# Optimization experiments

Measured on AMD Instinct MI355X. Metric: run time of the kernel, lower is better.

Reference implementation:

```python
import jax, jax.numpy as jnp
import numpy as np

L = 4


def make_coord(h, w):
    # pixel-center coords in [-1,1], shape (h*w, 2), dim order (y, x)
    ys = -1.0 + 1.0 / h + (2.0 / h) * jnp.arange(h, dtype=jnp.float32)
    xs = -1.0 + 1.0 / w + (2.0 / w) * jnp.arange(w, dtype=jnp.float32)
    gy, gx = jnp.meshgrid(ys, xs, indexing='ij')
    return jnp.stack([gy, gx], axis=-1).reshape(-1, 2)


def bilinear_sample(feat, gx, gy):
    # feat: (B,C,H,W); gx,gy in [-1,1], shape (B,N); align_corners=True
    B, C, H, W = feat.shape
    ix = (gx + 1.0) * 0.5 * (W - 1)
    iy = (gy + 1.0) * 0.5 * (H - 1)
    x0f = jnp.floor(ix)
    y0f = jnp.floor(iy)
    x0 = jnp.clip(x0f.astype(jnp.int32), 0, W - 1)
    x1 = jnp.clip(x0 + 1, 0, W - 1)
    y0 = jnp.clip(y0f.astype(jnp.int32), 0, H - 1)
    y1 = jnp.clip(y0 + 1, 0, H - 1)
    wx1 = ix - x0f
    wx0 = 1.0 - wx1
    wy1 = iy - y0f
    wy0 = 1.0 - wy1
    featf = feat.reshape(B, C, H * W)

    def g(yi, xi):
        idx = yi * W + xi  # (B,N)
        return jnp.take_along_axis(featf, idx[:, None, :], axis=2)  # (B,C,N)

    out = (g(y0, x0) * (wy0 * wx0)[:, None, :] + g(y0, x1) * (wy0 * wx1)[:, None, :]
           + g(y1, x0) * (wy1 * wx0)[:, None, :] + g(y1, x1) * (wy1 * wx1)[:, None, :])
    return out.transpose(0, 2, 1)  # (B,N,C)


def pos_enc(x):
    # x: (B,N,2) -> (B,N,4L); per dim: [sin_0..sin_{L-1}, cos_0..cos_{L-1}]
    freq = (2.0 ** jnp.arange(L, dtype=jnp.float32)) * np.pi
    spec = x[..., None] * freq  # (B,N,2,L)
    enc = jnp.concatenate([jnp.sin(spec), jnp.cos(spec)], axis=-1)  # (B,N,2,2L)
    return enc.reshape(*x.shape[:-1], 4 * L)


def mlp(x, w0, b0, w1, b1, w2, b2, w3, b3):
    h = jax.nn.relu(x @ w0 + b0)
    h = jax.nn.relu(h @ w1 + b1)
    h = jax.nn.relu(h @ w2 + b2)
    return h @ w3 + b3


def setup_inputs() -> dict:
    key = jax.random.key(0)
    ks = jax.random.split(key, 8)
    B, C, H, W = 4, 64, 128, 128
    hid, out_dim = 256, 3
    in_dim = C + 2 + 4 * L + 2  # 84
    s = 0.05
    return {
        'inp': jax.random.normal(ks[0], (B, C, H, W), jnp.float32),
        'w0': jax.random.normal(ks[1], (in_dim, hid), jnp.float32) * s,
        'b0': jnp.zeros((hid,), jnp.float32),
        'w1': jax.random.normal(ks[2], (hid, hid), jnp.float32) * s,
        'b1': jnp.zeros((hid,), jnp.float32),
        'w2': jax.random.normal(ks[3], (hid, hid), jnp.float32) * s,
        'b2': jnp.zeros((hid,), jnp.float32),
        'w3': jax.random.normal(ks[4], (hid, out_dim), jnp.float32) * s,
        'b3': jnp.zeros((out_dim,), jnp.float32),
        'scale': 2,
    }


def reference(inp, w0, b0, w1, b1, w2, b2, w3, b3, scale):
    B, C, H, W = inp.shape
    th, tw = int(round(H * scale)), int(round(W * scale))
    N = th * tw
    coord = jnp.broadcast_to(make_coord(th, tw)[None], (B, N, 2))
    # cell = (2/th, 2/tw); rel_cell = cell * (H, W)
    rel_cell = jnp.broadcast_to(
        jnp.array([2.0 / th * H, 2.0 / tw * W], jnp.float32), (B, N, 2))
    # feature-pixel coordinate map, appended as extra channels so one gather serves both
    fc = make_coord(H, W).reshape(H, W, 2).transpose(2, 0, 1)  # (2,H,W)
    aug = jnp.concatenate([inp, jnp.broadcast_to(fc[None], (B, 2, H, W))], axis=1)

    pe = pos_enc(coord)  # same for all 4 ensemble branches
    hw_scale = jnp.array([H, W], jnp.float32)
    rx, ry = 1.0 / H, 1.0 / W
    eps = 1e-6

    preds, areas = [], []
    for vx in (-1, 1):
        for vy in (-1, 1):
            c0 = jnp.clip(coord[..., 0] + vx * rx + eps, -1 + 1e-6, 1 - 1e-6)
            c1 = jnp.clip(coord[..., 1] + vy * ry + eps, -1 + 1e-6, 1 - 1e-6)
            # grid_sample uses (x, y) = flipped coord -> gx=c1, gy=c0
            q = bilinear_sample(aug, c1, c0)  # (B,N,C+2)
            q_feat, q_coord = q[..., :C], q[..., C:]
            rel = (coord - q_coord) * hw_scale  # (B,N,2)
            x = jnp.concatenate([q_feat, rel, pe, rel_cell], axis=-1)
            preds.append(mlp(x, w0, b0, w1, b1, w2, b2, w3, b3))
            areas.append(jnp.abs(rel[..., 0] * rel[..., 1]) + 1e-9)

    areas = [areas[3], areas[2], areas[1], areas[0]]  # diagonal swap
    tot = areas[0] + areas[1] + areas[2] + areas[3]
    ret = sum(p * (a / tot)[..., None] for p, a in zip(preds, areas))  # (B,N,out)
    return ret.reshape(B, th, tw, -1).transpose(0, 3, 1, 2)  # (B,out,th,tw)
```

## Files before the change

kernel.cpp:

```cpp
#include <hip/hip_runtime.h>
#include <math.h>

#define NB 4
#define NH 128
#define NW 128
#define TH 256
#define TW 256
#define K0 96
#define MROWS 256
#define PIXB 64

typedef _Float16 f16;
typedef f16  f16x8 __attribute__((ext_vector_type(8)));
typedef f16  f16x4v __attribute__((ext_vector_type(4)));
typedef float f32x4 __attribute__((ext_vector_type(4)));
typedef float f32x16 __attribute__((ext_vector_type(16)));

#define OFF_W1 24576
#define OFF_W2 (OFF_W1 + 65536)
#define OFF_W3 (OFF_W2 + 65536)
#define OFF_PE (OFF_W3 + 4096)
#define WS_W_ELEMS (OFF_PE + 4096)
#define FT_ELEMS (NB * NH * NW * 64)

__device__ __forceinline__ int act_off(int row, int colByte) {
  return row * 512 + (colByte ^ ((row & 7) << 4));
}

__device__ __forceinline__ void gload_lds16(const f16* g, f16* l) {
  __builtin_amdgcn_global_load_lds(
      (const __attribute__((address_space(1))) void*)(g),
      (__attribute__((address_space(3))) void*)(l), 16, 0, 0);
}

__global__ void cvt_weights(const float* __restrict__ w0, const float* __restrict__ w1,
                            const float* __restrict__ w2, const float* __restrict__ w3,
                            f16* __restrict__ ws) {
  const int i = blockIdx.x * 256 + threadIdx.x;
  if (i < 24576) {
    const int n = i / 96, k = i - n * 96;
    ws[i] = (k < 84) ? (f16)w0[k * 256 + n] : (f16)0.f;
  } else if (i < OFF_W2) {
    const int j = i - OFF_W1; const int n = j >> 8, k = j & 255;
    ws[i] = (f16)w1[k * 256 + n];
  } else if (i < OFF_W3) {
    const int j = i - OFF_W2; const int n = j >> 8, k = j & 255;
    ws[i] = (f16)w2[k * 256 + n];
  } else if (i < OFF_PE) {
    const int j = i - OFF_W3; const int n = j >> 8, k = j & 255;
    ws[i] = (n < 3) ? (f16)w3[k * 3 + n] : (f16)0.f;
  } else if (i < WS_W_ELEMS) {
    const int j = i - OFF_PE;
    const int o = (j & 2047) >> 3, e = j & 7;
    const float c = (2.0f * o + 1.0f) / 256.0f - 1.0f;
    const float f = (float)(1 << (e & 3)) * (float)M_PI;
    ws[i] = (f16)((e < 4) ? sinf(c * f) : cosf(c * f));
  }
}

__global__ void transpose_feat(const float* __restrict__ feat, f16* __restrict__ ft) {
  __shared__ f16 tile[64][66];
  const int bid = blockIdx.x;
  const int xt = bid & 1, y = (bid >> 1) & 127, b = bid >> 8;
  const int x0 = xt * 64;
  {
    const int c4 = threadIdx.x >> 6, x = threadIdx.x & 63;
#pragma unroll
    for (int co = 0; co < 16; ++co) {
      const int c = co * 4 + c4;
      tile[x][c] = (f16)feat[((size_t)(b * 64 + c) * NH + y) * NW + x0 + x];
    }
  }
  __syncthreads();
  {
    const int x4 = threadIdx.x >> 6, c = threadIdx.x & 63;
#pragma unroll
    for (int xo = 0; xo < 16; ++xo) {
      const int x = xo * 4 + x4;
      ft[((size_t)(b * NH + y) * NW + x0 + x) * 64 + c] = tile[x][c];
    }
  }
}

template<int K>
__device__ __forceinline__ void dense_layer(const f16* __restrict__ Wt,
                                            const float* __restrict__ bias,
                                            char* actc, f16* wlds,
                                            int wm, int wn, int l, int tid) {
  constexpr int NK = K / 16, NP = NK / 2;
  const int lo = l & 31, hi = l >> 5;
  const int sn = tid & 255, sh = tid >> 8;
  const f16* src = Wt + (size_t)sn * K + sh * 8;
  f16* wdst = wlds + sh * 2048 + ((tid >> 6) & 3) * 512;
  const int aoff = (wn * 64 + lo) * 8;
  const int brow0 = wm * 128 + lo;

  f32x16 acc[2][4];
#pragma unroll
  for (int nt = 0; nt < 2; ++nt) {
    f32x16 ci;
#pragma unroll
    for (int g = 0; g < 4; ++g) {
      const float4 b4 = *(const float4*)(bias + wn * 64 + nt * 32 + 8 * g + 4 * hi);
      ci[4 * g + 0] = b4.x; ci[4 * g + 1] = b4.y; ci[4 * g + 2] = b4.z; ci[4 * g + 3] = b4.w;
    }
#pragma unroll
    for (int mt = 0; mt < 4; ++mt) acc[nt][mt] = ci;
  }

  gload_lds16(src + 0 * 16, wdst + 0 * 4096);
  gload_lds16(src + 1 * 16, wdst + 1 * 4096);
  asm volatile("s_waitcnt vmcnt(0)" ::: "memory");
  __builtin_amdgcn_s_barrier();
  asm volatile("" ::: "memory");

#pragma unroll
  for (int p = 0; p < NP; ++p) {
    const int s0 = 2 * p, s1 = 2 * p + 1;
    if (p + 1 < NP) {
      gload_lds16(src + (s0 + 2) * 16, wdst + ((s0 + 2) & 3) * 4096);
      gload_lds16(src + (s1 + 2) * 16, wdst + ((s1 + 2) & 3) * 4096);
    }
    const f16* wb0 = wlds + (s0 & 3) * 4096 + hi * 2048 + aoff;
    const f16x8 A00 = *(const f16x8*)(wb0);
    const f16x8 A01 = *(const f16x8*)(wb0 + 256);
    const f16x8 B00 = *(const f16x8*)(actc + act_off(brow0 + 0 * 32, s0 * 32 + hi * 16));
    const f16x8 B01 = *(const f16x8*)(actc + act_off(brow0 + 1 * 32, s0 * 32 + hi * 16));
    const f16x8 B02 = *(const f16x8*)(actc + act_off(brow0 + 2 * 32, s0 * 32 + hi * 16));
    const f16x8 B03 = *(const f16x8*)(actc + act_off(brow0 + 3 * 32, s0 * 32 + hi * 16));
    const f16* wb1 = wlds + (s1 & 3) * 4096 + hi * 2048 + aoff;
    const f16x8 A10 = *(const f16x8*)(wb1);
    const f16x8 A11 = *(const f16x8*)(wb1 + 256);
    const f16x8 B10 = *(const f16x8*)(actc + act_off(brow0 + 0 * 32, s1 * 32 + hi * 16));
    const f16x8 B11 = *(const f16x8*)(actc + act_off(brow0 + 1 * 32, s1 * 32 + hi * 16));
    const f16x8 B12 = *(const f16x8*)(actc + act_off(brow0 + 2 * 32, s1 * 32 + hi * 16));
    const f16x8 B13 = *(const f16x8*)(actc + act_off(brow0 + 3 * 32, s1 * 32 + hi * 16));

    asm volatile("s_waitcnt lgkmcnt(6)" ::: "memory");
    __builtin_amdgcn_sched_barrier(0);
    __builtin_amdgcn_s_setprio(1);
    acc[0][0] = __builtin_amdgcn_mfma_f32_32x32x16_f16(A00, B00, acc[0][0], 0, 0, 0);
    acc[0][1] = __builtin_amdgcn_mfma_f32_32x32x16_f16(A00, B01, acc[0][1], 0, 0, 0);
    acc[0][2] = __builtin_amdgcn_mfma_f32_32x32x16_f16(A00, B02, acc[0][2], 0, 0, 0);
    acc[0][3] = __builtin_amdgcn_mfma_f32_32x32x16_f16(A00, B03, acc[0][3], 0, 0, 0);
    acc[1][0] = __builtin_amdgcn_mfma_f32_32x32x16_f16(A01, B00, acc[1][0], 0, 0, 0);
    acc[1][1] = __builtin_amdgcn_mfma_f32_32x32x16_f16(A01, B01, acc[1][1], 0, 0, 0);
    acc[1][2] = __builtin_amdgcn_mfma_f32_32x32x16_f16(A01, B02, acc[1][2], 0, 0, 0);
    acc[1][3] = __builtin_amdgcn_mfma_f32_32x32x16_f16(A01, B03, acc[1][3], 0, 0, 0);
    __builtin_amdgcn_s_setprio(0);

    asm volatile("s_waitcnt lgkmcnt(0)" ::: "memory");
    __builtin_amdgcn_sched_barrier(0);
    __builtin_amdgcn_s_setprio(1);
    acc[0][0] = __builtin_amdgcn_mfma_f32_32x32x16_f16(A10, B10, acc[0][0], 0, 0, 0);
    acc[0][1] = __builtin_amdgcn_mfma_f32_32x32x16_f16(A10, B11, acc[0][1], 0, 0, 0);
    acc[0][2] = __builtin_amdgcn_mfma_f32_32x32x16_f16(A10, B12, acc[0][2], 0, 0, 0);
    acc[0][3] = __builtin_amdgcn_mfma_f32_32x32x16_f16(A10, B13, acc[0][3], 0, 0, 0);
    acc[1][0] = __builtin_amdgcn_mfma_f32_32x32x16_f16(A11, B10, acc[1][0], 0, 0, 0);
    acc[1][1] = __builtin_amdgcn_mfma_f32_32x32x16_f16(A11, B11, acc[1][1], 0, 0, 0);
    acc[1][2] = __builtin_amdgcn_mfma_f32_32x32x16_f16(A11, B12, acc[1][2], 0, 0, 0);
    acc[1][3] = __builtin_amdgcn_mfma_f32_32x32x16_f16(A11, B13, acc[1][3], 0, 0, 0);
    __builtin_amdgcn_s_setprio(0);

    if (p + 1 < NP)
      asm volatile("s_waitcnt vmcnt(0)" ::: "memory");
    __builtin_amdgcn_s_barrier();
    asm volatile("" ::: "memory");
  }

#pragma unroll
  for (int nt = 0; nt < 2; ++nt)
#pragma unroll
    for (int mt = 0; mt < 4; ++mt)
#pragma unroll
      for (int g = 0; g < 4; ++g) {
        f16x4v o;
        o[0] = (f16)fmaxf(acc[nt][mt][4 * g + 0], 0.f);
        o[1] = (f16)fmaxf(acc[nt][mt][4 * g + 1], 0.f);
        o[2] = (f16)fmaxf(acc[nt][mt][4 * g + 2], 0.f);
        o[3] = (f16)fmaxf(acc[nt][mt][4 * g + 3], 0.f);
        const int row = wm * 128 + mt * 32 + lo;
        const int colB = wn * 128 + nt * 64 + 16 * g + 8 * hi;
        *(f16x4v*)(actc + act_off(row, colB)) = o;
      }
}

template<bool USE_FT>
__global__ __launch_bounds__(512, 2) void inr2d_mfma(
    const float* __restrict__ feat, const f16* __restrict__ ft,
    const float* __restrict__ b0, const float* __restrict__ b1,
    const float* __restrict__ b2, const float* __restrict__ b3,
    const f16* __restrict__ ws, float* __restrict__ out)
{
  __shared__ f16 act[MROWS * 256];
  __shared__ f16 wlds[4 * 4096];
  f16 (*pred_s)[4] = (f16(*)[4])wlds;

  char* actc = (char*)act;
  const int t = threadIdx.x;
  const int blk = ((blockIdx.x & 7) << 9) | (blockIdx.x >> 3);

  {
    const int r = t >> 1, sub = t & 1;
    const int pix = r >> 2, e = r & 3;
    const int gp = blk * PIXB + pix;
    const int b = gp >> 16, rem = gp & 65535;
    const int oy = rem >> 8, ox = rem & 255;

    const float cy = (2.0f * oy + 1.0f) / (float)TH - 1.0f;
    const float cx = (2.0f * ox + 1.0f) / (float)TW - 1.0f;
    const float vx = (e & 2) ? 1.0f : -1.0f;
    const float vy = (e & 1) ? 1.0f : -1.0f;
    const float rr = 1.0f / (float)NH;

    float c0 = fminf(fmaxf(cy + vx * rr + 1e-6f, -1.0f + 1e-6f), 1.0f - 1e-6f);
    float c1 = fminf(fmaxf(cx + vy * rr + 1e-6f, -1.0f + 1e-6f), 1.0f - 1e-6f);

    const float ix = (c1 + 1.0f) * 0.5f * (float)(NW - 1);
    const float iy = (c0 + 1.0f) * 0.5f * (float)(NH - 1);
    const float x0f = floorf(ix), y0f = floorf(iy);
    int x0 = (int)x0f; x0 = max(0, min(x0, NW - 1));
    int x1 = min(x0 + 1, NW - 1);
    int y0 = (int)y0f; y0 = max(0, min(y0, NH - 1));
    int y1 = min(y0 + 1, NH - 1);
    const float wx1 = ix - x0f, wx0 = 1.0f - wx1;
    const float wy1 = iy - y0f, wy0 = 1.0f - wy1;
    const float w00 = wy0 * wx0, w01 = wy0 * wx1, w10 = wy1 * wx0, w11 = wy1 * wx1;

    if (USE_FT) {
      const f16* fb = ft + (size_t)b * (NH * NW * 64);
      const f16* r00 = fb + (size_t)(y0 * NW + x0) * 64 + sub * 32;
      const f16* r01 = fb + (size_t)(y0 * NW + x1) * 64 + sub * 32;
      const f16* r10 = fb + (size_t)(y1 * NW + x0) * 64 + sub * 32;
      const f16* r11 = fb + (size_t)(y1 * NW + x1) * 64 + sub * 32;
#pragma unroll
      for (int h = 0; h < 4; ++h) {
        const f16x8 a00 = *(const f16x8*)(r00 + h * 8);
        const f16x8 a01 = *(const f16x8*)(r01 + h * 8);
        const f16x8 a10 = *(const f16x8*)(r10 + h * 8);
        const f16x8 a11 = *(const f16x8*)(r11 + h * 8);
        f16x8 o;
#pragma unroll
        for (int i = 0; i < 8; ++i) {
          o[i] = (f16)(w00 * (float)a00[i] + w01 * (float)a01[i] +
                       w10 * (float)a10[i] + w11 * (float)a11[i]);
        }
        *(f16x8*)(actc + act_off(r, 64 * sub + 16 * h)) = o;
      }
    } else {
      const float* fb = feat + (size_t)b * 64 * NH * NW;
      const int i00 = y0 * NW + x0, i01 = y0 * NW + x1;
      const int i10 = y1 * NW + x0, i11 = y1 * NW + x1;
#pragma unroll
      for (int i = 0; i < 32; ++i) {
        const int c = sub * 32 + i;
        const float* fc = fb + (size_t)c * (NH * NW);
        const float v = w00 * fc[i00] + w01 * fc[i01] + w10 * fc[i10] + w11 * fc[i11];
        *(f16*)(actc + act_off(r, 2 * c)) = (f16)v;
      }
    }
    if (sub == 0) {
      const float qy = -1.0f + 1.0f / NH + (2.0f / NH) * (wy0 * (float)y0 + wy1 * (float)y1);
      const float qx = -1.0f + 1.0f / NW + (2.0f / NW) * (wx0 * (float)x0 + wx1 * (float)x1);
      const float rely = (cy - qy) * (float)NH;
      const float relx = (cx - qx) * (float)NW;
      *(f16*)(actc + act_off(r, 2 * 64)) = (f16)rely;
      *(f16*)(actc + act_off(r, 2 * 65)) = (f16)relx;
      if (USE_FT) {
        const f16* py = ws + OFF_PE + (size_t)oy * 8;
        const f16* px = ws + OFF_PE + 2048 + (size_t)ox * 8;
#pragma unroll
        for (int j = 0; j < 8; ++j) {
          *(f16*)(actc + act_off(r, 2 * (66 + j))) = py[j];
          *(f16*)(actc + act_off(r, 2 * (74 + j))) = px[j];
        }
      } else {
#pragma unroll
        for (int ll = 0; ll < 4; ++ll) {
          const float f = (float)(1 << ll) * (float)M_PI;
          *(f16*)(actc + act_off(r, 2 * (66 + ll))) = (f16)sinf(cy * f);
          *(f16*)(actc + act_off(r, 2 * (70 + ll))) = (f16)cosf(cy * f);
          *(f16*)(actc + act_off(r, 2 * (74 + ll))) = (f16)sinf(cx * f);
          *(f16*)(actc + act_off(r, 2 * (78 + ll))) = (f16)cosf(cx * f);
        }
      }
      *(f16*)(actc + act_off(r, 2 * 82)) = (f16)1.0f;
      *(f16*)(actc + act_off(r, 2 * 83)) = (f16)1.0f;
#pragma unroll
      for (int z = 84; z < K0; ++z) *(f16*)(actc + act_off(r, 2 * z)) = (f16)0.f;
    }
  }
  __syncthreads();

  const int w = t >> 6, l = t & 63;
  const int wm = w >> 2, wn = w & 3;

  dense_layer<K0 >(ws,          b0, actc, wlds, wm, wn, l, t);
  __syncthreads();
  dense_layer<256>(ws + OFF_W1, b1, actc, wlds, wm, wn, l, t);
  __syncthreads();
  dense_layer<256>(ws + OFF_W2, b2, actc, wlds, wm, wn, l, t);
  __syncthreads();

  {
    const int nl = l & 15, kq = l >> 4;
    const f16* Abase = ws + OFF_W3 + nl * 256 + kq * 8;
#pragma unroll
    for (int p = 0; p < 2; ++p) {
      const int row = w * 32 + p * 16 + nl;
      f32x4 acc = {0.f, 0.f, 0.f, 0.f};
#pragma unroll
      for (int ks = 0; ks < 8; ++ks) {
        f16x8 a = *(const f16x8*)(Abase + ks * 32);
        f16x8 b = *(const f16x8*)(actc + act_off(row, 64 * ks + 16 * kq));
        acc = __builtin_amdgcn_mfma_f32_16x16x32_f16(a, b, acc, 0, 0, 0);
      }
      if (l < 16) {
        f16x4v pr;
        pr[0] = (f16)(acc[0] + b3[0]); pr[1] = (f16)(acc[1] + b3[1]);
        pr[2] = (f16)(acc[2] + b3[2]); pr[3] = (f16)0.f;
        *(f16x4v*)(&pred_s[w * 32 + p * 16 + l][0]) = pr;
      }
    }
  }
  __syncthreads();

  if (t < PIXB * 3) {
    const int pix = t / 3, o = t - pix * 3;
    const int gp = blk * PIXB + pix;
    const int b = gp >> 16, rem = gp & 65535;
    const int oy = rem >> 8, ox = rem & 255;
    const float cy = (2.0f * oy + 1.0f) / (float)TH - 1.0f;
    const float cx = (2.0f * ox + 1.0f) / (float)TW - 1.0f;
    const float rr = 1.0f / (float)NH;
    float ar[4];
#pragma unroll
    for (int e = 0; e < 4; ++e) {
      const float vx = (e & 2) ? 1.0f : -1.0f;
      const float vy = (e & 1) ? 1.0f : -1.0f;
      float c0 = fminf(fmaxf(cy + vx * rr + 1e-6f, -1.0f + 1e-6f), 1.0f - 1e-6f);
      float c1 = fminf(fmaxf(cx + vy * rr + 1e-6f, -1.0f + 1e-6f), 1.0f - 1e-6f);
      const float ix = (c1 + 1.0f) * 0.5f * (float)(NW - 1);
      const float iy = (c0 + 1.0f) * 0.5f * (float)(NH - 1);
      const float x0f = floorf(ix), y0f = floorf(iy);
      int x0 = (int)x0f; x0 = max(0, min(x0, NW - 1));
      int x1 = min(x0 + 1, NW - 1);
      int y0 = (int)y0f; y0 = max(0, min(y0, NH - 1));
      int y1 = min(y0 + 1, NH - 1);
      const float wx1 = ix - x0f, wx0 = 1.0f - wx1;
      const float wy1 = iy - y0f, wy0 = 1.0f - wy1;
      const float qy = -1.0f + 1.0f / NH + (2.0f / NH) * (wy0 * (float)y0 + wy1 * (float)y1);
      const float qx = -1.0f + 1.0f / NW + (2.0f / NW) * (wx0 * (float)x0 + wx1 * (float)x1);
      const float rely = (cy - qy) * (float)NH;
      const float relx = (cx - qx) * (float)NW;
      ar[e] = fabsf(rely * relx) + 1e-9f;
    }
    const int r0 = pix * 4;
    const float tot = ar[0] + ar[1] + ar[2] + ar[3];
    const float v = (float)pred_s[r0][o] * ar[3] + (float)pred_s[r0 + 1][o] * ar[2] +
                    (float)pred_s[r0 + 2][o] * ar[1] + (float)pred_s[r0 + 3][o] * ar[0];
    out[(((size_t)b * 3 + o) << 16) + (oy << 8) + ox] = v / tot;
  }
}

extern "C" void kernel_launch(void* const* d_in, const int* in_sizes, int n_in,
                              void* d_out, int out_size, void* d_ws, size_t ws_size,
                              hipStream_t stream) {
  const float* feat = (const float*)d_in[0];
  const float* w0 = (const float*)d_in[1];
  const float* b0 = (const float*)d_in[2];
  const float* w1 = (const float*)d_in[3];
  const float* b1 = (const float*)d_in[4];
  const float* w2 = (const float*)d_in[5];
  const float* b2 = (const float*)d_in[6];
  const float* w3 = (const float*)d_in[7];
  const float* b3 = (const float*)d_in[8];
  float* out = (float*)d_out;
  f16* ws = (f16*)d_ws;

  cvt_weights<<<(WS_W_ELEMS + 255) / 256, 256, 0, stream>>>(w0, w1, w2, w3, ws);

  const int blocks = (NB * TH * TW) / PIXB;
  const bool use_ft = ws_size >= (size_t)(WS_W_ELEMS + FT_ELEMS) * sizeof(f16);
  if (use_ft) {
    f16* ft = ws + WS_W_ELEMS;
    transpose_feat<<<NB * NH * (NW / 64), 256, 0, stream>>>(feat, ft);
    inr2d_mfma<true><<<blocks, 512, 0, stream>>>(feat, ft, b0, b1, b2, b3, ws, out);
  } else {
    inr2d_mfma<false><<<blocks, 512, 0, stream>>>(feat, nullptr, b0, b1, b2, b3, ws, out);
  }
}
```

Before: 439.5 us.

## Use 256-thread blocks with 4 waves each computing 128x128 output tiles

Halves the block to 4 waves, each wave now owning a 128-row by 128-column tile (4x4 MFMA 32x32 accumulators) instead of 128x64, so each B fragment read from LDS is reused across four weight fragments. This reduces LDS activation reads per MFMA and the number of barrier participants. The gather stage is reassigned so one thread handles a full sample row, and the LDS swizzle is widened to XOR over 32 rows. In exchange, accumulator register pressure doubles (256 AGPR/VGPR for acc) and there are fewer waves per CU to hide latency.

```diff
diff --git a/kernel.cpp b/kernel.cpp
--- a/kernel.cpp
+++ b/kernel.cpp
@@ -24,7 +24,7 @@
 #define FT_ELEMS (NB * NH * NW * 64)
 
 __device__ __forceinline__ int act_off(int row, int colByte) {
-  return row * 512 + (colByte ^ ((row & 7) << 4));
+  return row * 512 + (colByte ^ ((row & 31) << 4));
 }
 
 __device__ __forceinline__ void gload_lds16(const f16* g, f16* l) {
@@ -89,27 +89,28 @@
                                             int wm, int wn, int l, int tid) {
   constexpr int NK = K / 16, NP = NK / 2;
   const int lo = l & 31, hi = l >> 5;
-  const int sn = tid & 255, sh = tid >> 8;
-  const f16* src = Wt + (size_t)sn * K + sh * 8;
-  f16* wdst = wlds + sh * 2048 + ((tid >> 6) & 3) * 512;
-  const int aoff = (wn * 64 + lo) * 8;
+  const f16* src = Wt + (size_t)tid * K;
+  f16* wdstw = wlds + (tid >> 6) * 512;
+  const int aoff = (wn * 128 + lo) * 8;
   const int brow0 = wm * 128 + lo;
 
-  f32x16 acc[2][4];
-#pragma unroll
-  for (int nt = 0; nt < 2; ++nt) {
+  f32x16 acc[4][4];
+#pragma unroll
+  for (int nt = 0; nt < 4; ++nt) {
     f32x16 ci;
 #pragma unroll
     for (int g = 0; g < 4; ++g) {
-      const float4 b4 = *(const float4*)(bias + wn * 64 + nt * 32 + 8 * g + 4 * hi);
+      const float4 b4 = *(const float4*)(bias + wn * 128 + nt * 32 + 8 * g + 4 * hi);
       ci[4 * g + 0] = b4.x; ci[4 * g + 1] = b4.y; ci[4 * g + 2] = b4.z; ci[4 * g + 3] = b4.w;
     }
 #pragma unroll
     for (int mt = 0; mt < 4; ++mt) acc[nt][mt] = ci;
   }
 
-  gload_lds16(src + 0 * 16, wdst + 0 * 4096);
-  gload_lds16(src + 1 * 16, wdst + 1 * 4096);
+  gload_lds16(src + 0 * 16 + 0, wdstw + 0 * 4096 + 0);
+  gload_lds16(src + 0 * 16 + 8, wdstw + 0 * 4096 + 2048);
+  gload_lds16(src + 1 * 16 + 0, wdstw + 1 * 4096 + 0);
+  gload_lds16(src + 1 * 16 + 8, wdstw + 1 * 4096 + 2048);
   asm volatile("s_waitcnt vmcnt(0)" ::: "memory");
   __builtin_amdgcn_s_barrier();
   asm volatile("" ::: "memory");
@@ -118,48 +119,54 @@
   for (int p = 0; p < NP; ++p) {
     const int s0 = 2 * p, s1 = 2 * p + 1;
     if (p + 1 < NP) {
-      gload_lds16(src + (s0 + 2) * 16, wdst + ((s0 + 2) & 3) * 4096);
-      gload_lds16(src + (s1 + 2) * 16, wdst + ((s1 + 2) & 3) * 4096);
+      gload_lds16(src + (s0 + 2) * 16 + 0, wdstw + ((s0 + 2) & 3) * 4096 + 0);
+      gload_lds16(src + (s0 + 2) * 16 + 8, wdstw + ((s0 + 2) & 3) * 4096 + 2048);
+      gload_lds16(src + (s1 + 2) * 16 + 0, wdstw + ((s1 + 2) & 3) * 4096 + 0);
+      gload_lds16(src + (s1 + 2) * 16 + 8, wdstw + ((s1 + 2) & 3) * 4096 + 2048);
     }
     const f16* wb0 = wlds + (s0 & 3) * 4096 + hi * 2048 + aoff;
-    const f16x8 A00 = *(const f16x8*)(wb0);
-    const f16x8 A01 = *(const f16x8*)(wb0 + 256);
+    const f16x8 A00 = *(const f16x8*)(wb0 + 0 * 256);
+    const f16x8 A01 = *(const f16x8*)(wb0 + 1 * 256);
+    const f16x8 A02 = *(const f16x8*)(wb0 + 2 * 256);
+    const f16x8 A03 = *(const f16x8*)(wb0 + 3 * 256);
     const f16x8 B00 = *(const f16x8*)(actc + act_off(brow0 + 0 * 32, s0 * 32 + hi * 16));
     const f16x8 B01 = *(const f16x8*)(actc + act_off(brow0 + 1 * 32, s0 * 32 + hi * 16));
     const f16x8 B02 = *(const f16x8*)(actc + act_off(brow0 + 2 * 32, s0 * 32 + hi * 16));
     const f16x8 B03 = *(const f16x8*)(actc + act_off(brow0 + 3 * 32, s0 * 32 + hi * 16));
     const f16* wb1 = wlds + (s1 & 3) * 4096 + hi * 2048 + aoff;
-    const f16x8 A10 = *(const f16x8*)(wb1);
-    const f16x8 A11 = *(const f16x8*)(wb1 + 256);
+    const f16x8 A10 = *(const f16x8*)(wb1 + 0 * 256);
+    const f16x8 A11 = *(const f16x8*)(wb1 + 1 * 256);
+    const f16x8 A12 = *(const f16x8*)(wb1 + 2 * 256);
+    const f16x8 A13 = *(const f16x8*)(wb1 + 3 * 256);
     const f16x8 B10 = *(const f16x8*)(actc + act_off(brow0 + 0 * 32, s1 * 32 + hi * 16));
     const f16x8 B11 = *(const f16x8*)(actc + act_off(brow0 + 1 * 32, s1 * 32 + hi * 16));
     const f16x8 B12 = *(const f16x8*)(actc + act_off(brow0 + 2 * 32, s1 * 32 + hi * 16));
     const f16x8 B13 = *(const f16x8*)(actc + act_off(brow0 + 3 * 32, s1 * 32 + hi * 16));
 
-    asm volatile("s_waitcnt lgkmcnt(6)" ::: "memory");
+    asm volatile("s_waitcnt lgkmcnt(8)" ::: "memory");
     __builtin_amdgcn_sched_barrier(0);
     __builtin_amdgcn_s_setprio(1);
-    acc[0][0] = __builtin_amdgcn_mfma_f32_32x32x16_f16(A00, B00, acc[0][0], 0, 0, 0);
-    acc[0][1] = __builtin_amdgcn_mfma_f32_32x32x16_f16(A00, B01, acc[0][1], 0, 0, 0);
-    acc[0][2] = __builtin_amdgcn_mfma_f32_32x32x16_f16(A00, B02, acc[0][2], 0, 0, 0);
-    acc[0][3] = __builtin_amdgcn_mfma_f32_32x32x16_f16(A00, B03, acc[0][3], 0, 0, 0);
-    acc[1][0] = __builtin_amdgcn_mfma_f32_32x32x16_f16(A01, B00, acc[1][0], 0, 0, 0);
-    acc[1][1] = __builtin_amdgcn_mfma_f32_32x32x16_f16(A01, B01, acc[1][1], 0, 0, 0);
-    acc[1][2] = __builtin_amdgcn_mfma_f32_32x32x16_f16(A01, B02, acc[1][2], 0, 0, 0);
-    acc[1][3] = __builtin_amdgcn_mfma_f32_32x32x16_f16(A01, B03, acc[1][3], 0, 0, 0);
+#pragma unroll
+    for (int nt = 0; nt < 4; ++nt) {
+      const f16x8 A = (nt == 0) ? A00 : (nt == 1) ? A01 : (nt == 2) ? A02 : A03;
+      acc[nt][0] = __builtin_amdgcn_mfma_f32_32x32x16_f16(A, B00, acc[nt][0], 0, 0, 0);
+      acc[nt][1] = __builtin_amdgcn_mfma_f32_32x32x16_f16(A, B01, acc[nt][1], 0, 0, 0);
+      acc[nt][2] = __builtin_amdgcn_mfma_f32_32x32x16_f16(A, B02, acc[nt][2], 0, 0, 0);
+      acc[nt][3] = __builtin_amdgcn_mfma_f32_32x32x16_f16(A, B03, acc[nt][3], 0, 0, 0);
+    }
     __builtin_amdgcn_s_setprio(0);
 
     asm volatile("s_waitcnt lgkmcnt(0)" ::: "memory");
     __builtin_amdgcn_sched_barrier(0);
     __builtin_amdgcn_s_setprio(1);
-    acc[0][0] = __builtin_amdgcn_mfma_f32_32x32x16_f16(A10, B10, acc[0][0], 0, 0, 0);
-    acc[0][1] = __builtin_amdgcn_mfma_f32_32x32x16_f16(A10, B11, acc[0][1], 0, 0, 0);
-    acc[0][2] = __builtin_amdgcn_mfma_f32_32x32x16_f16(A10, B12, acc[0][2], 0, 0, 0);
-    acc[0][3] = __builtin_amdgcn_mfma_f32_32x32x16_f16(A10, B13, acc[0][3], 0, 0, 0);
-    acc[1][0] = __builtin_amdgcn_mfma_f32_32x32x16_f16(A11, B10, acc[1][0], 0, 0, 0);
-    acc[1][1] = __builtin_amdgcn_mfma_f32_32x32x16_f16(A11, B11, acc[1][1], 0, 0, 0);
-    acc[1][2] = __builtin_amdgcn_mfma_f32_32x32x16_f16(A11, B12, acc[1][2], 0, 0, 0);
-    acc[1][3] = __builtin_amdgcn_mfma_f32_32x32x16_f16(A11, B13, acc[1][3], 0, 0, 0);
+#pragma unroll
+    for (int nt = 0; nt < 4; ++nt) {
+      const f16x8 A = (nt == 0) ? A10 : (nt == 1) ? A11 : (nt == 2) ? A12 : A13;
+      acc[nt][0] = __builtin_amdgcn_mfma_f32_32x32x16_f16(A, B10, acc[nt][0], 0, 0, 0);
+      acc[nt][1] = __builtin_amdgcn_mfma_f32_32x32x16_f16(A, B11, acc[nt][1], 0, 0, 0);
+      acc[nt][2] = __builtin_amdgcn_mfma_f32_32x32x16_f16(A, B12, acc[nt][2], 0, 0, 0);
+      acc[nt][3] = __builtin_amdgcn_mfma_f32_32x32x16_f16(A, B13, acc[nt][3], 0, 0, 0);
+    }
     __builtin_amdgcn_s_setprio(0);
 
     if (p + 1 < NP)
@@ -169,7 +176,7 @@
   }
 
 #pragma unroll
-  for (int nt = 0; nt < 2; ++nt)
+  for (int nt = 0; nt < 4; ++nt)
 #pragma unroll
     for (int mt = 0; mt < 4; ++mt)
 #pragma unroll
@@ -180,13 +187,13 @@
         o[2] = (f16)fmaxf(acc[nt][mt][4 * g + 2], 0.f);
         o[3] = (f16)fmaxf(acc[nt][mt][4 * g + 3], 0.f);
         const int row = wm * 128 + mt * 32 + lo;
-        const int colB = wn * 128 + nt * 64 + 16 * g + 8 * hi;
+        const int colB = wn * 256 + nt * 64 + 16 * g + 8 * hi;
         *(f16x4v*)(actc + act_off(row, colB)) = o;
       }
 }
 
 template<bool USE_FT>
-__global__ __launch_bounds__(512, 2) void inr2d_mfma(
+__global__ __launch_bounds__(256, 1) void inr2d_mfma(
     const float* __restrict__ feat, const f16* __restrict__ ft,
     const float* __restrict__ b0, const float* __restrict__ b1,
     const float* __restrict__ b2, const float* __restrict__ b3,
@@ -201,7 +208,7 @@
   const int blk = ((blockIdx.x & 7) << 9) | (blockIdx.x >> 3);
 
   {
-    const int r = t >> 1, sub = t & 1;
+    const int r = t;
     const int pix = r >> 2, e = r & 3;
     const int gp = blk * PIXB + pix;
     const int b = gp >> 16, rem = gp & 65535;
@@ -229,12 +236,12 @@
 
     if (USE_FT) {
       const f16* fb = ft + (size_t)b * (NH * NW * 64);
-      const f16* r00 = fb + (size_t)(y0 * NW + x0) * 64 + sub * 32;
-      const f16* r01 = fb + (size_t)(y0 * NW + x1) * 64 + sub * 32;
-      const f16* r10 = fb + (size_t)(y1 * NW + x0) * 64 + sub * 32;
-      const f16* r11 = fb + (size_t)(y1 * NW + x1) * 64 + sub * 32;
-#pragma unroll
-      for (int h = 0; h < 4; ++h) {
+      const f16* r00 = fb + (size_t)(y0 * NW + x0) * 64;
+      const f16* r01 = fb + (size_t)(y0 * NW + x1) * 64;
+      const f16* r10 = fb + (size_t)(y1 * NW + x0) * 64;
+      const f16* r11 = fb + (size_t)(y1 * NW + x1) * 64;
+#pragma unroll
+      for (int h = 0; h < 8; ++h) {
         const f16x8 a00 = *(const f16x8*)(r00 + h * 8);
         const f16x8 a01 = *(const f16x8*)(r01 + h * 8);
         const f16x8 a10 = *(const f16x8*)(r10 + h * 8);
@@ -245,21 +252,20 @@
           o[i] = (f16)(w00 * (float)a00[i] + w01 * (float)a01[i] +
                        w10 * (float)a10[i] + w11 * (float)a11[i]);
         }
-        *(f16x8*)(actc + act_off(r, 64 * sub + 16 * h)) = o;
+        *(f16x8*)(actc + act_off(r, 16 * h)) = o;
       }
     } else {
       const float* fb = feat + (size_t)b * 64 * NH * NW;
       const int i00 = y0 * NW + x0, i01 = y0 * NW + x1;
       const int i10 = y1 * NW + x0, i11 = y1 * NW + x1;
 #pragma unroll
-      for (int i = 0; i < 32; ++i) {
-        const int c = sub * 32 + i;
+      for (int c = 0; c < 64; ++c) {
         const float* fc = fb + (size_t)c * (NH * NW);
         const float v = w00 * fc[i00] + w01 * fc[i01] + w10 * fc[i10] + w11 * fc[i11];
         *(f16*)(actc + act_off(r, 2 * c)) = (f16)v;
       }
     }
-    if (sub == 0) {
+    {
       const float qy = -1.0f + 1.0f / NH + (2.0f / NH) * (wy0 * (float)y0 + wy1 * (float)y1);
       const float qx = -1.0f + 1.0f / NW + (2.0f / NW) * (wx0 * (float)x0 + wx1 * (float)x1);
       const float rely = (cy - qy) * (float)NH;
@@ -293,7 +299,7 @@
   __syncthreads();
 
   const int w = t >> 6, l = t & 63;
-  const int wm = w >> 2, wn = w & 3;
+  const int wm = w >> 1, wn = w & 1;
 
   dense_layer<K0 >(ws,          b0, actc, wlds, wm, wn, l, t);
   __syncthreads();
@@ -306,8 +312,8 @@
     const int nl = l & 15, kq = l >> 4;
     const f16* Abase = ws + OFF_W3 + nl * 256 + kq * 8;
 #pragma unroll
-    for (int p = 0; p < 2; ++p) {
-      const int row = w * 32 + p * 16 + nl;
+    for (int p = 0; p < 4; ++p) {
+      const int row = w * 64 + p * 16 + nl;
       f32x4 acc = {0.f, 0.f, 0.f, 0.f};
 #pragma unroll
       for (int ks = 0; ks < 8; ++ks) {
@@ -319,7 +325,7 @@
         f16x4v pr;
         pr[0] = (f16)(acc[0] + b3[0]); pr[1] = (f16)(acc[1] + b3[1]);
         pr[2] = (f16)(acc[2] + b3[2]); pr[3] = (f16)0.f;
-        *(f16x4v*)(&pred_s[w * 32 + p * 16 + l][0]) = pr;
+        *(f16x4v*)(&pred_s[w * 64 + p * 16 + l][0]) = pr;
       }
     }
   }
@@ -385,8 +391,8 @@
   if (use_ft) {
     f16* ft = ws + WS_W_ELEMS;
     transpose_feat<<<NB * NH * (NW / 64), 256, 0, stream>>>(feat, ft);
-    inr2d_mfma<true><<<blocks, 512, 0, stream>>>(feat, ft, b0, b1, b2, b3, ws, out);
+    inr2d_mfma<true><<<blocks, 256, 0, stream>>>(feat, ft, b0, b1, b2, b3, ws, out);
   } else {
-    inr2d_mfma<false><<<blocks, 512, 0, stream>>>(feat, nullptr, b0, b1, b2, b3, ws, out);
-  }
-}
+    inr2d_mfma<false><<<blocks, 256, 0, stream>>>(feat, nullptr, b0, b1, b2, b3, ws, out);
+  }
+}
```

Measured after the change: 516.3 us. +17.5%, slower.
